# Kernel tuning notes

Measured on AMD Instinct MI355X. Metric: run time of the kernel, lower is better.

Reference implementation:

```python
import jax, jax.numpy as jnp
import numpy as np

VOCAB, FEAT, EMB, HID, AFF = 10000, 512, 256, 512, 512
B, T, HW = 32, 60, 14


def setup_inputs() -> dict:
    key = jax.random.key(0)
    ks = jax.random.split(key, 16)
    s = lambda k, shape, fan: jax.random.normal(k, shape, jnp.float32) * (1.0 / np.sqrt(fan))
    return {
        "cnn_feat": jax.random.normal(ks[0], (B, FEAT, HW, HW), jnp.float32),
        "captions": jax.random.randint(ks[1], (B, T), 0, VOCAB),
        "Wk": s(ks[2], (AFF, HID), HID),          # attention affine_k
        "Wv": s(ks[3], (AFF, FEAT), FEAT),        # attention affine_v
        "wa": s(ks[4], (AFF,), AFF),              # attention affine (out dim 1)
        "embed_table": jax.random.normal(ks[5], (VOCAB, EMB), jnp.float32),
        "Wh": s(ks[6], (HID, FEAT), FEAT), "bh": jnp.zeros((HID,), jnp.float32),
        "Wc": s(ks[7], (HID, FEAT), FEAT), "bc": jnp.zeros((HID,), jnp.float32),
        "Wih": s(ks[8], (4 * HID, EMB + FEAT), EMB + FEAT),
        "Whh": s(ks[9], (4 * HID, HID), HID),
        "bih": jnp.zeros((4 * HID,), jnp.float32),
        "bhh": jnp.zeros((4 * HID,), jnp.float32),
        "Wfc": s(ks[10], (VOCAB, HID), HID), "bfc": jnp.zeros((VOCAB,), jnp.float32),
    }


def _forward(cnn_feat, captions, Wk, Wv, wa, embed_table, Wh, bh, Wc, bc,
             Wih, Whh, bih, bhh, Wfc, bfc):
    Bs, C = cnn_feat.shape[0], cnn_feat.shape[1]
    feats = cnn_feat.reshape(Bs, C, -1).transpose(0, 2, 1)   # [B, P, FEAT]
    g = cnn_feat.mean(axis=(2, 3))                           # [B, FEAT]
    h0 = g @ Wh.T + bh
    c0 = g @ Wc.T + bc
    kv = jnp.einsum('bpc,ac->bpa', feats, Wv)                # affine_v(v), step-invariant
    emb = embed_table[captions]                              # [B, T, EMB]

    def step(carry, e_t):
        h, c = carry
        # additive attention: tanh(affine_k(h) + affine_v(v)) @ wa
        z = jnp.tanh((h @ Wk.T)[:, None, :] + kv) @ wa       # [B, P]
        alpha = jax.nn.softmax(z, axis=1)
        ctx = jnp.einsum('bp,bpc->bc', alpha, feats)         # [B, FEAT]
        x = jnp.concatenate([e_t, ctx], axis=1)
        gates = x @ Wih.T + bih + h @ Whh.T + bhh
        i, f, gg, o = jnp.split(gates, 4, axis=1)
        c = jax.nn.sigmoid(f) * c + jax.nn.sigmoid(i) * jnp.tanh(gg)
        h = jax.nn.sigmoid(o) * jnp.tanh(c)
        logit = h @ Wfc.T + bfc                              # dropout = identity (eval)
        return (h, c), logit

    _, logits = jax.lax.scan(step, (h0, c0), emb.transpose(1, 0, 2))
    return logits.transpose(1, 0, 2)                         # [B, T, VOCAB]


def reference(cnn_feat, captions, Wk, Wv, wa, embed_table, Wh, bh, Wc, bc,
              Wih, Whh, bih, bhh, Wfc, bfc):
    return _forward(cnn_feat, captions, Wk, Wv, wa, embed_table, Wh, bh, Wc, bc,
                    Wih, Whh, bih, bhh, Wfc, bfc)
```

## Files before the change

kernel.cpp:

```cpp
#include <hip/hip_runtime.h>
#include <hip/hip_bf16.h>
#include <cstdint>
#include <cstddef>

#define VOCABN 10000
#define FEATC 512
#define EMBN 256
#define HIDN 512
#define AFFN 512
#define BB 32
#define TTN 60
#define PPN 196
#define GROWS 2048

using bf16 = __hip_bfloat16;

typedef __attribute__((ext_vector_type(8))) short short8;
typedef __attribute__((ext_vector_type(4))) float f32x4;

__device__ __forceinline__ float b2f(bf16 x){ return __bfloat162float(x); }
__device__ __forceinline__ float fexp2(float x){ return __builtin_amdgcn_exp2f(x); }
__device__ __forceinline__ float frcp(float x){ return __builtin_amdgcn_rcpf(x); }
__device__ __forceinline__ float fsig(float x){ return frcp(1.f + fexp2(-1.4426950408889634f*x)); }
__device__ __forceinline__ float ftanhf(float x){ return 1.f - 2.f*frcp(1.f + fexp2(2.8853900817779268f*x)); }

__device__ __forceinline__ float aload(const float* p){
  return __hip_atomic_load((float*)p, __ATOMIC_RELAXED, __HIP_MEMORY_SCOPE_AGENT);
}
__device__ __forceinline__ void astore(float* p, float v){
  __hip_atomic_store(p, v, __ATOMIC_RELAXED, __HIP_MEMORY_SCOPE_AGENT);
}
__device__ __forceinline__ void astoreu(unsigned* p, unsigned v){
  __hip_atomic_store(p, v, __ATOMIC_RELAXED, __HIP_MEMORY_SCOPE_AGENT);
}
__device__ __forceinline__ unsigned aloadu(const unsigned* p){
  return __hip_atomic_load((unsigned*)p, __ATOMIC_RELAXED, __HIP_MEMORY_SCOPE_AGENT);
}

__device__ __forceinline__ f32x4 ic_load4(const float* p){
  f32x4 r;
  asm volatile("global_load_dwordx4 %0, %1, off sc0 sc1" : "=&v"(r) : "v"(p));
  return r;
}
__device__ __forceinline__ void ic_store4(float* p, f32x4 v){
  asm volatile("global_store_dwordx4 %0, %1, off sc0 sc1" :: "v"(p), "v"(v) : "memory");
}
__device__ __forceinline__ void ic_wait(){
  asm volatile("s_waitcnt vmcnt(0)" ::: "memory");
  __builtin_amdgcn_sched_barrier(0);
}

__device__ __forceinline__ void unpack8(uint4 u, float* f){
  f[0] = __uint_as_float(u.x << 16); f[1] = __uint_as_float(u.x & 0xffff0000u);
  f[2] = __uint_as_float(u.y << 16); f[3] = __uint_as_float(u.y & 0xffff0000u);
  f[4] = __uint_as_float(u.z << 16); f[5] = __uint_as_float(u.z & 0xffff0000u);
  f[6] = __uint_as_float(u.w << 16); f[7] = __uint_as_float(u.w & 0xffff0000u);
}

__global__ void __launch_bounds__(256) k_probe(const uint32_t* __restrict__ w, int* __restrict__ flag,
                                               unsigned* __restrict__ flags){
  __shared__ int s;
  if (threadIdx.x == 0) s = 0;
  __syncthreads();
  int hit = 0;
  for (int i = threadIdx.x; i < 32768; i += 256){
    uint32_t v = w[i];
    if (((v & 0x7F800000u) == 0x7F800000u) || ((v & 0x00007F80u) == 0x00007F80u)) hit = 1;
  }
  if (hit) atomicOr(&s, 1);
  for (int i = threadIdx.x; i < 1024; i += 256) astoreu(&flags[i], 0u);
  __syncthreads();
  if (threadIdx.x == 0) flag[0] = s;
}

__global__ void __launch_bounds__(256) k_cvt(const void* __restrict__ src, bf16* __restrict__ dst,
                                             int nquad, const int* __restrict__ flag){
  bool f32 = flag[0] != 0;
  int stride = gridDim.x * 256;
  for (int i = blockIdx.x*256 + threadIdx.x; i < nquad; i += stride){
    if (f32){
      float4 v = reinterpret_cast<const float4*>(src)[i];
      bf16* d = dst + 4*(size_t)i;
      d[0] = __float2bfloat16(v.x); d[1] = __float2bfloat16(v.y);
      d[2] = __float2bfloat16(v.z); d[3] = __float2bfloat16(v.w);
    } else {
      reinterpret_cast<uint2*>(dst)[i] = reinterpret_cast<const uint2*>(src)[i];
    }
  }
}

__global__ void __launch_bounds__(256) k_transpose(const bf16* __restrict__ cnn, bf16* __restrict__ feats){
  __shared__ bf16 tile[32][34];
  int ct = blockIdx.x, pt = blockIdx.y, b = blockIdx.z;
  int tid = threadIdx.x;
  int lc = tid >> 5, lp = tid & 31;
  int p = pt*32 + lp;
  #pragma unroll
  for (int i=0;i<4;i++){
    int cc = ct*32 + lc + i*8;
    bf16 v = __float2bfloat16(0.f);
    if (p < PPN) v = cnn[((size_t)b*FEATC + cc)*PPN + p];
    tile[lc + i*8][lp] = v;
  }
  __syncthreads();
  #pragma unroll
  for (int i=0;i<4;i++){
    int pp = pt*32 + lc + i*8;
    if (pp < PPN) feats[((size_t)b*PPN + pp)*FEATC + ct*32 + lp] = tile[lp][lc + i*8];
  }
}

__global__ void __launch_bounds__(256) k_wkt(const bf16* __restrict__ W, bf16* __restrict__ WT){
  __shared__ bf16 tile[32][33];
  const int c0 = blockIdx.x*32, r0 = blockIdx.y*32;
  const int lc = threadIdx.x >> 5, lp = threadIdx.x & 31;
  #pragma unroll
  for (int i=0;i<4;i++) tile[lc + i*8][lp] = W[(size_t)(r0 + lc + i*8)*HIDN + c0 + lp];
  __syncthreads();
  #pragma unroll
  for (int i=0;i<4;i++) WT[(size_t)(c0 + lc + i*8)*HIDN + r0 + lp] = tile[lp][lc + i*8];
}

__global__ void __launch_bounds__(256) k_wcat2(const bf16* __restrict__ Wih, const bf16* __restrict__ Whh,
      const bf16* __restrict__ bih, const bf16* __restrict__ bhh,
      bf16* __restrict__ Weh, bf16* __restrict__ Wctx, float* __restrict__ biasCat){
  const int rloc = threadIdx.x >> 5, lane32 = threadIdx.x & 31;
  const int r = blockIdx.x*8 + rloc;
  const int j = r >> 2, g = r & 3;
  const int src = g*HIDN + j;
  for (int e4 = lane32; e4 < 192; e4 += 32){
    const int e = e4*4;
    uint2 v = (e < 256) ? *reinterpret_cast<const uint2*>(Wih + (size_t)src*768 + e)
                        : *reinterpret_cast<const uint2*>(Whh + (size_t)src*HIDN + (e - 256));
    *reinterpret_cast<uint2*>(Weh + (size_t)r*768 + e) = v;
  }
  for (int e4 = lane32; e4 < 128; e4 += 32){
    const int e = e4*4;
    *reinterpret_cast<uint2*>(Wctx + (size_t)r*512 + e) =
        *reinterpret_cast<const uint2*>(Wih + (size_t)src*768 + 256 + e);
  }
  if (lane32 == 0) biasCat[r] = b2f(bih[src]) + b2f(bhh[src]);
}

__global__ void __launch_bounds__(256) k_init(const bf16* __restrict__ cnn,
      const bf16* __restrict__ Wh, const bf16* __restrict__ bh,
      const bf16* __restrict__ Wc, const bf16* __restrict__ bc,
      float* __restrict__ h, float* __restrict__ c){
  __shared__ float gl[FEATC];
  int b = blockIdx.x, tid = threadIdx.x;
  for (int cc = tid; cc < FEATC; cc += 256){
    const bf16* src = cnn + ((size_t)b*FEATC + cc)*PPN;
    const uint2* sp = reinterpret_cast<const uint2*>(src);
    float acc = 0.f;
    for (int q=0;q<PPN/4;q++){
      uint2 u = sp[q];
      acc += __uint_as_float(u.x<<16) + __uint_as_float(u.x&0xffff0000u)
           + __uint_as_float(u.y<<16) + __uint_as_float(u.y&0xffff0000u);
    }
    gl[cc] = acc * (1.0f/196.0f);
  }
  __syncthreads();
  for (int i = tid; i < HIDN; i += 256){
    const uint4* wr1 = reinterpret_cast<const uint4*>(Wh + (size_t)i*FEATC);
    const uint4* wr2 = reinterpret_cast<const uint4*>(Wc + (size_t)i*FEATC);
    float a1 = 0.f, a2 = 0.f;
    #pragma unroll 4
    for (int k8=0; k8<FEATC/8; k8++){
      float w1[8], w2[8];
      unpack8(wr1[k8], w1); unpack8(wr2[k8], w2);
      const float* gp = &gl[k8*8];
      #pragma unroll
      for (int j=0;j<8;j++){ a1 = fmaf(w1[j], gp[j], a1); a2 = fmaf(w2[j], gp[j], a2); }
    }
    astore(&h[b*HIDN+i], a1 + b2f(bh[i]));
    astore(&c[b*HIDN+i], a2 + b2f(bc[i]));
  }
}

__global__ void __launch_bounds__(512) k_hk0(const bf16* __restrict__ WkT,
      const float* __restrict__ h, float* __restrict__ part){
  __shared__ float hl[64];
  const int tid = threadIdx.x;
  const int k = blockIdx.x & 7, b = blockIdx.x >> 3;
  if (tid < 64) hl[tid] = aload(&h[b*HIDN + k*64 + tid]);
  __syncthreads();
  const bf16* wp = WkT + (size_t)(k*64)*AFFN + tid;
  float acc = 0.f;
  #pragma unroll 8
  for (int j=0; j<64; j++) acc = fmaf(b2f(wp[(size_t)j*AFFN]), hl[j], acc);
  astore(&part[((size_t)(b*8 + k))*AFFN + tid], acc);
}

template<int OUTMODE, bool BIAS, bool NT>
__global__ void __launch_bounds__(256) gemm_bt(const bf16* __restrict__ A, const bf16* __restrict__ Bw,
        const bf16* __restrict__ bias, void* __restrict__ Cout, int M, int N, int K,
        const int* __restrict__ flag){
  __shared__ __align__(16) bf16 As[64][40];
  __shared__ __align__(16) bf16 Bs[64][40];
  int tid = threadIdx.x;
  int m0 = blockIdx.y*64, n0 = blockIdx.x*64;
  int lr = tid >> 2;
  int lk = (tid & 3)*8;
  int wave = tid >> 6, lane = tid & 63;
  int ml = lane & 15, kg = lane >> 4;
  f32x4 acc0 = {0.f,0.f,0.f,0.f}, acc1 = acc0, acc2 = acc0, acc3 = acc0;
  for (int k0=0; k0<K; k0+=32){
    __syncthreads();
    {
      uint4 av = *reinterpret_cast<const uint4*>(A + (size_t)(m0+lr)*K + k0 + lk);
      *reinterpret_cast<uint4*>(&As[lr][lk]) = av;
      uint4 bv = make_uint4(0u,0u,0u,0u);
      int bn = n0 + lr;
      if (bn < N) bv = *reinterpret_cast<const uint4*>(Bw + (size_t)bn*K + k0 + lk);
      *reinterpret_cast<uint4*>(&Bs[lr][lk]) = bv;
    }
    __syncthreads();
    short8 af = *reinterpret_cast<const short8*>(&As[wave*16 + ml][kg*8]);
    short8 b0 = *reinterpret_cast<const short8*>(&Bs[ 0 + ml][kg*8]);
    short8 b1 = *reinterpret_cast<const short8*>(&Bs[16 + ml][kg*8]);
    short8 b2 = *reinterpret_cast<const short8*>(&Bs[32 + ml][kg*8]);
    short8 b3 = *reinterpret_cast<const short8*>(&Bs[48 + ml][kg*8]);
    acc0 = __builtin_amdgcn_mfma_f32_16x16x32_bf16(af, b0, acc0, 0,0,0);
    acc1 = __builtin_amdgcn_mfma_f32_16x16x32_bf16(af, b1, acc1, 0,0,0);
    acc2 = __builtin_amdgcn_mfma_f32_16x16x32_bf16(af, b2, acc2, 0,0,0);
    acc3 = __builtin_amdgcn_mfma_f32_16x16x32_bf16(af, b3, acc3, 0,0,0);
  }
  bool of32;
  if (OUTMODE == 0) of32 = true;
  else if (OUTMODE == 2) of32 = false;
  else of32 = (flag[0] != 0);
  int mb = m0 + wave*16 + (lane>>4)*4;
  int cl = lane & 15;
  f32x4 av[4] = {acc0, acc1, acc2, acc3};
  #pragma unroll
  for (int j=0;j<4;j++){
    int n = n0 + j*16 + cl;
    if (n < N){
      float bv = BIAS ? b2f(bias[n]) : 0.f;
      #pragma unroll
      for (int rr=0; rr<4; rr++){
        float v = av[j][rr] + bv;
        if (of32){
          float* p = &((float*)Cout)[(size_t)(mb+rr)*N + n];
          if (NT) __builtin_nontemporal_store(v, p); else *p = v;
        } else {
          bf16 hv = __float2bfloat16(v);
          short sv = *reinterpret_cast<short*>(&hv);
          short* p = reinterpret_cast<short*>(&((bf16*)Cout)[(size_t)(mb+rr)*N + n]);
          if (NT) __builtin_nontemporal_store(sv, p); else *p = sv;
        }
      }
    }
  }
}

__global__ void __launch_bounds__(256) gemm_gb(const bf16* __restrict__ A, const bf16* __restrict__ BwAll,
        bf16* __restrict__ Gout){
  const bf16* Bw = BwAll + (size_t)blockIdx.z*PPN*FEATC;
  bf16* Cout = Gout + (size_t)blockIdx.z*GROWS*PPN;
  __shared__ __align__(16) bf16 As[64][40];
  __shared__ __align__(16) bf16 Bs[64][40];
  int tid = threadIdx.x;
  int m0 = blockIdx.y*64, n0 = blockIdx.x*64;
  int lr = tid >> 2;
  int lk = (tid & 3)*8;
  int wave = tid >> 6, lane = tid & 63;
  int ml = lane & 15, kg = lane >> 4;
  f32x4 acc0 = {0.f,0.f,0.f,0.f}, acc1 = acc0, acc2 = acc0, acc3 = acc0;
  for (int k0=0; k0<FEATC; k0+=32){
    __syncthreads();
    {
      uint4 av = *reinterpret_cast<const uint4*>(A + (size_t)(m0+lr)*FEATC + k0 + lk);
      *reinterpret_cast<uint4*>(&As[lr][lk]) = av;
      uint4 bv = make_uint4(0u,0u,0u,0u);
      int bn = n0 + lr;
      if (bn < PPN) bv = *reinterpret_cast<const uint4*>(Bw + (size_t)bn*FEATC + k0 + lk);
      *reinterpret_cast<uint4*>(&Bs[lr][lk]) = bv;
    }
    __syncthreads();
    short8 af = *reinterpret_cast<const short8*>(&As[wave*16 + ml][kg*8]);
    short8 b0 = *reinterpret_cast<const short8*>(&Bs[ 0 + ml][kg*8]);
    short8 b1 = *reinterpret_cast<const short8*>(&Bs[16 + ml][kg*8]);
    short8 b2 = *reinterpret_cast<const short8*>(&Bs[32 + ml][kg*8]);
    short8 b3 = *reinterpret_cast<const short8*>(&Bs[48 + ml][kg*8]);
    acc0 = __builtin_amdgcn_mfma_f32_16x16x32_bf16(af, b0, acc0, 0,0,0);
    acc1 = __builtin_amdgcn_mfma_f32_16x16x32_bf16(af, b1, acc1, 0,0,0);
    acc2 = __builtin_amdgcn_mfma_f32_16x16x32_bf16(af, b2, acc2, 0,0,0);
    acc3 = __builtin_amdgcn_mfma_f32_16x16x32_bf16(af, b3, acc3, 0,0,0);
  }
  int mb = m0 + wave*16 + (lane>>4)*4;
  int cl = lane & 15;
  f32x4 av[4] = {acc0, acc1, acc2, acc3};
  #pragma unroll
  for (int j=0;j<4;j++){
    int n = n0 + j*16 + cl;
    if (n < PPN){
      #pragma unroll
      for (int rr=0; rr<4; rr++)
        Cout[(size_t)(mb+rr)*PPN + n] = __float2bfloat16(av[j][rr]);
    }
  }
}

__device__ __forceinline__ void fbar_signal(unsigned* f8, int myk, unsigned token){
  asm volatile("s_waitcnt vmcnt(0)" ::: "memory");
  __syncthreads();
  if (threadIdx.x == 0) astoreu(&f8[myk], token);
}
__device__ __forceinline__ void fbar_wait(unsigned* f8, unsigned token){
  const int lane = threadIdx.x & 63;
  unsigned guard = 0;
  for (;;){
    unsigned v = (lane < 8) ? aloadu(&f8[lane]) : token;
    if (__all((int)(v >= token))) break;
    if (++guard > 50000000u) break;
    __builtin_amdgcn_s_sleep(1);
  }
  __syncthreads();
}

__device__ __forceinline__ void gacc(const bf16* w, const float* x, int len,
                                     float& a0, float& a1, float& a2, float& a3){
  #pragma unroll 4
  for (int e=0; e<len; e+=8){
    float w8[8]; unpack8(*reinterpret_cast<const uint4*>(w+e), w8);
    float4 x0 = *reinterpret_cast<const float4*>(x+e);
    float4 x1 = *reinterpret_cast<const float4*>(x+e+4);
    a0 = fmaf(w8[0],x0.x,a0); a1 = fmaf(w8[1],x0.y,a1);
    a2 = fmaf(w8[2],x0.z,a2); a3 = fmaf(w8[3],x0.w,a3);
    a0 = fmaf(w8[4],x1.x,a0); a1 = fmaf(w8[5],x1.y,a1);
    a2 = fmaf(w8[6],x1.z,a2); a3 = fmaf(w8[7],x1.w,a3);
  }
}

__global__ void __launch_bounds__(512) k_pers(
    const bf16* __restrict__ kvB, const bf16* __restrict__ WkT,
    const bf16* __restrict__ Weh, const bf16* __restrict__ Gglob,
    const float* __restrict__ biasCat, const bf16* __restrict__ wa,
    const bf16* __restrict__ table, const int* __restrict__ captions,
    float* __restrict__ hstate, const float* __restrict__ cinit,
    float* __restrict__ part,
    float* __restrict__ zarr,
    bf16* __restrict__ Hb, unsigned* __restrict__ flags)
{
  extern __shared__ __align__(16) char dynsm[];
  bf16* kv_s = reinterpret_cast<bf16*>(dynsm);
  bf16* G_s  = reinterpret_cast<bf16*>(dynsm + 25600);
  __shared__ __align__(16) float xs[768];
  __shared__ __align__(16) float hks[512];
  __shared__ __align__(16) float als[200];
  __shared__ __align__(16) float gs[256];
  __shared__ __align__(16) float zes[32];
  __shared__ __align__(16) float hnew[64];

  const int tid = threadIdx.x;
  const int bid = blockIdx.x;
  const int k = bid & 7, b = bid >> 3;
  unsigned* fl = flags + b*32;
  const int np = (k < 4) ? 25 : 24;
  const int p0 = (k < 4) ? k*25 : 100 + (k-4)*24;
  const int lane = tid & 63, wv = tid >> 6;

  const int r2 = tid >> 1, half = tid & 1;
  const int rowg = k*256 + r2;

  {
    const uint4* src = reinterpret_cast<const uint4*>(kvB + ((size_t)(b*PPN + p0))*AFFN);
    uint4* dst = reinterpret_cast<uint4*>(kv_s);
    for (int i = tid; i < np*64; i += 512) dst[i] = src[i];
  }
  {
    const uint2* src = reinterpret_cast<const uint2*>(Gglob + ((size_t)(b*GROWS) + k*256)*PPN);
    uint2* dst = reinterpret_cast<uint2*>(G_s);
    for (int i = tid; i < 12544; i += 512) dst[i] = src[i];
  }
  float creg = 0.f;
  if (tid < 64) creg = cinit[b*HIDN + k*64 + tid];
  float wf[8];
  unpack8(*reinterpret_cast<const uint4*>(wa + lane*8), wf);
  __syncthreads();

  for (int t = 0; t < TTN; t++){
    f32x4 pq[8]; f32x4 hq;
    if (tid < 128){
      const float* pp = part + (size_t)b*8*AFFN + tid*4;
      #pragma unroll
      for (int kk=0;kk<8;kk++) pq[kk] = ic_load4(pp + (size_t)kk*AFFN);
    } else if (tid < 256){
      hq = ic_load4(hstate + (size_t)b*HIDN + (tid-128)*4);
    } else {
      const int tok = captions[b*TTN + t];
      xs[tid-256] = b2f(table[(size_t)tok*EMBN + (tid-256)]);
    }
    ic_wait();
    if (tid < 128){
      f32x4 s = pq[0];
      #pragma unroll
      for (int kk=1;kk<8;kk++) s += pq[kk];
      *reinterpret_cast<f32x4*>(&hks[tid*4]) = s;
    } else if (tid < 256){
      *reinterpret_cast<f32x4*>(&xs[256 + (tid-128)*4]) = hq;
    }
    __syncthreads();

    {
      float hf[8];
      const float4* hp = reinterpret_cast<const float4*>(&hks[lane*8]);
      float4 t0 = hp[0], t1 = hp[1];
      hf[0]=t0.x; hf[1]=t0.y; hf[2]=t0.z; hf[3]=t0.w;
      hf[4]=t1.x; hf[5]=t1.y; hf[6]=t1.z; hf[7]=t1.w;
      for (int pl = wv; pl < np; pl += 8){
        float kf[8]; unpack8(*reinterpret_cast<const uint4*>(kv_s + pl*512 + lane*8), kf);
        float acc = wf[0]*ftanhf(kf[0]+hf[0]) + wf[1]*ftanhf(kf[1]+hf[1])
                  + wf[2]*ftanhf(kf[2]+hf[2]) + wf[3]*ftanhf(kf[3]+hf[3])
                  + wf[4]*ftanhf(kf[4]+hf[4]) + wf[5]*ftanhf(kf[5]+hf[5])
                  + wf[6]*ftanhf(kf[6]+hf[6]) + wf[7]*ftanhf(kf[7]+hf[7]);
        #pragma unroll
        for (int s=1;s<64;s<<=1) acc += __shfl_xor(acc, s, 64);
        if (lane == 0) zes[pl] = acc;
      }
    }
    __syncthreads();
    if (tid < 8) ic_store4(&zarr[(size_t)(b*8+k)*32 + tid*4],
                           *reinterpret_cast<f32x4*>(&zes[tid*4]));

    fbar_signal(fl, k, (unsigned)(2*t+1));

    float a0=0.f,a1=0.f,a2=0.f,a3=0.f;
    gacc(Weh + (size_t)rowg*768 + half*384, xs + half*384, 384, a0,a1,a2,a3);

    fbar_wait(fl, (unsigned)(2*t+1));

    f32x4 zq;
    if (tid < 64) zq = ic_load4(&zarr[(size_t)b*256 + tid*4]);
    ic_wait();
    if (tid < 64){
      const int kk2 = tid >> 3, i0 = (tid & 7)*4;
      const int npk = (kk2 < 4) ? 25 : 24;
      const int p0k = (kk2 < 4) ? kk2*25 : 100 + (kk2-4)*24;
      #pragma unroll
      for (int jj=0;jj<4;jj++) if (i0+jj < npk) als[p0k+i0+jj] = zq[jj];
    }
    __syncthreads();
    if (wv == 0){
      float m = -1e30f;
      for (int i=lane;i<PPN;i+=64) m = fmaxf(m, als[i]);
      #pragma unroll
      for (int s=1;s<64;s<<=1) m = fmaxf(m, __shfl_xor(m, s, 64));
      float ssum = 0.f;
      for (int i=lane;i<PPN;i+=64){
        float e = fexp2((als[i]-m)*1.4426950408889634f);
        als[i] = e; ssum += e;
      }
      #pragma unroll
      for (int s=1;s<64;s<<=1) ssum += __shfl_xor(ssum, s, 64);
      float inv = 1.0f/ssum;
      for (int i=lane;i<PPN;i+=64) als[i] *= inv;
    }
    __syncthreads();

    float ga = 0.f;
    {
      const uint32_t* gr = reinterpret_cast<const uint32_t*>(G_s + r2*PPN + half*98);
      const float* ap = als + half*98;
      #pragma unroll 7
      for (int i=0;i<49;i++){
        uint32_t u = gr[i];
        ga = fmaf(__uint_as_float(u << 16),          ap[2*i],   ga);
        ga = fmaf(__uint_as_float(u & 0xffff0000u),  ap[2*i+1], ga);
      }
    }
    {
      float acc = (a0+a1)+(a2+a3) + ga;
      acc += __shfl_xor(acc, 1, 64);
      if (half == 0) gs[r2] = acc + biasCat[rowg];
    }
    __syncthreads();

    if (tid < 64){
      const int j = k*64 + tid;
      float gi = gs[tid*4+0], gf = gs[tid*4+1], gg = gs[tid*4+2], go = gs[tid*4+3];
      float cn = fsig(gf)*creg + fsig(gi)*ftanhf(gg);
      float hn = fsig(go)*ftanhf(cn);
      creg = cn;
      hnew[tid] = hn;
      Hb[((size_t)b*TTN + t)*HIDN + j] = __float2bfloat16(hn);
    }
    __syncthreads();
    if (tid < 16) ic_store4(&hstate[(size_t)b*HIDN + k*64 + tid*4],
                            *reinterpret_cast<f32x4*>(&hnew[tid*4]));

    {
      const bf16* wp = WkT + (size_t)(k*64)*AFFN + tid;
      float acc = 0.f;
      #pragma unroll 8
      for (int j=0;j<64;j++) acc = fmaf(b2f(wp[(size_t)j*AFFN]), hnew[j], acc);
      hks[tid] = acc;
    }
    __syncthreads();
    if (tid < 128) ic_store4(&part[((size_t)(b*8+k))*AFFN + tid*4],
                             *reinterpret_cast<f32x4*>(&hks[tid*4]));

    fbar_signal(fl, k, (unsigned)(2*t+2));
    fbar_wait(fl, (unsigned)(2*t+2));
  }
}

static inline int cvt_grid(int nquad){ int g = (nquad + 255)/256; return g > 1024 ? 1024 : g; }

extern "C" void kernel_launch(void* const* d_in, const int* in_sizes, int n_in,
                              void* d_out, int out_size, void* d_ws, size_t ws_size,
                              hipStream_t stream) {
  const int* captions = (const int*)d_in[1];
  char* ws = (char*)d_ws;

  bf16*  feats  = (bf16*) (ws + 0);
  bf16*  kvB    = (bf16*) (ws + 6422528);
  float* hstate = (float*)(ws + 12845056);
  float* cstate = (float*)(ws + 12910592);
  float* part   = (float*)(ws + 12976128);
  float* zarr   = (float*)(ws + 13500416);
  unsigned* flags=(unsigned*)(ws + 13533184);
  bf16*  Hb     = (bf16*) (ws + 13537280);
  bf16*  cnnB   = (bf16*) (ws + 15503360);
  bf16*  WehB   = (bf16*) (ws + 15503360);
  bf16*  WctxB  = (bf16*) (ws + 18649088);
  bf16*  tableB = (bf16*) (ws + 21925888);
  bf16*  WkB    = (bf16*) (ws + 27045888);
  bf16*  WkTB   = (bf16*) (ws + 27570176);
  bf16*  WvB    = (bf16*) (ws + 28094464);
  bf16*  WhB    = (bf16*) (ws + 28618752);
  bf16*  WcB    = (bf16*) (ws + 29143040);
  bf16*  WihB   = (bf16*) (ws + 29667328);
  bf16*  WhhB   = (bf16*) (ws + 32813056);
  bf16*  WfcB   = (bf16*) (ws + 34910208);
  bf16*  waB    = (bf16*) (ws + 45150208);
  bf16*  bhB    = (bf16*) (ws + 45151232);
  bf16*  bcB    = (bf16*) (ws + 45152256);
  bf16*  bihB   = (bf16*) (ws + 45153280);
  bf16*  bhhB   = (bf16*) (ws + 45157376);
  bf16*  bfcB   = (bf16*) (ws + 45161472);
  float* biasCat= (float*)(ws + 45181472);
  int*   flag   = (int*)  (ws + 45189664);
  if (ws_size < 45189680ull) return;

  bf16* Gglob = (bf16*)d_out;

  k_probe<<<1, 256, 0, stream>>>((const uint32_t*)d_in[5], flag, flags);

  struct CvtJob { const void* src; bf16* dst; int n; };
  const CvtJob jobs[15] = {
    {d_in[0],  cnnB,   3211264}, {d_in[2],  WkB,  262144}, {d_in[3],  WvB,  262144},
    {d_in[4],  waB,    512},     {d_in[5],  tableB, 2560000},
    {d_in[6],  WhB,    262144},  {d_in[7],  bhB,  512},
    {d_in[8],  WcB,    262144},  {d_in[9],  bcB,  512},
    {d_in[10], WihB,   1572864}, {d_in[11], WhhB, 1048576},
    {d_in[12], bihB,   2048},    {d_in[13], bhhB, 2048},
    {d_in[14], WfcB,   5120000}, {d_in[15], bfcB, 10000},
  };
  for (int i = 0; i < 15; i++){
    int nq = jobs[i].n / 4;
    k_cvt<<<cvt_grid(nq), 256, 0, stream>>>(jobs[i].src, jobs[i].dst, nq, flag);
  }

  k_transpose<<<dim3(16,7,32), 256, 0, stream>>>(cnnB, feats);
  k_init<<<32, 256, 0, stream>>>(cnnB, WhB, bhB, WcB, bcB, hstate, cstate);
  k_wkt<<<dim3(16,16), 256, 0, stream>>>(WkB, WkTB);
  k_wcat2<<<256, 256, 0, stream>>>(WihB, WhhB, bihB, bhhB, WehB, WctxB, biasCat);
  k_hk0<<<256, 512, 0, stream>>>(WkTB, hstate, part);
  gemm_bt<2,false,false><<<dim3(8,98), 256, 0, stream>>>(feats, WvB, (const bf16*)nullptr,
                                                   (void*)kvB, 6272, 512, 512, (const int*)nullptr);
  gemm_gb<<<dim3(4,32,32), 256, 0, stream>>>(WctxB, feats, Gglob);

  k_pers<<<256, 512, 125952, stream>>>(kvB, WkTB, WehB, Gglob, biasCat, waB, tableB,
                                       captions, hstate, cstate, part, zarr, Hb, flags);

  gemm_bt<1,true,true><<<dim3(157,30), 256, 0, stream>>>(Hb, WfcB, bfcB, d_out,
                                                    1920, 10000, 512, flag);
}
```

Measured before the change: 1.557 ms.

## Precompute embedding gate contributions via batched GEMM and move h load off critical path

The embedding half of the LSTM input projection (emb @ Wih_emb^T plus biases) is hoisted out of the persistent recurrent kernel into a one-shot gather and GEMM over all timesteps. Inside the loop only the Whh part is computed per step, with the gate term for the next step prefetched from Gemb. The h-state reload is moved after the z reduction so it overlaps the barrier, and the Hb write is deferred past the flag signal. The 15 conversion launches are merged into one multi-job kernel, and the Wfc conversion is moved after the recurrent kernel so its workspace can be shared with Gemb. In exchange the biases and embedding gates are now rounded to bf16, and the workspace layout changes.

```diff
diff --git a/kernel.cpp b/kernel.cpp
--- a/kernel.cpp
+++ b/kernel.cpp
@@ -24,17 +24,17 @@
 __device__ __forceinline__ float fsig(float x){ return frcp(1.f + fexp2(-1.4426950408889634f*x)); }
 __device__ __forceinline__ float ftanhf(float x){ return 1.f - 2.f*frcp(1.f + fexp2(2.8853900817779268f*x)); }
 
+__device__ __forceinline__ void astore(float* p, float v){
+  __hip_atomic_store(p, v, __ATOMIC_RELAXED, __HIP_MEMORY_SCOPE_AGENT);
+}
+__device__ __forceinline__ void astoreu(unsigned* p, unsigned v){
+  __hip_atomic_store(p, v, __ATOMIC_RELAXED, __HIP_MEMORY_SCOPE_AGENT);
+}
+__device__ __forceinline__ unsigned aloadu(const unsigned* p){
+  return __hip_atomic_load((unsigned*)p, __ATOMIC_RELAXED, __HIP_MEMORY_SCOPE_AGENT);
+}
 __device__ __forceinline__ float aload(const float* p){
   return __hip_atomic_load((float*)p, __ATOMIC_RELAXED, __HIP_MEMORY_SCOPE_AGENT);
-}
-__device__ __forceinline__ void astore(float* p, float v){
-  __hip_atomic_store(p, v, __ATOMIC_RELAXED, __HIP_MEMORY_SCOPE_AGENT);
-}
-__device__ __forceinline__ void astoreu(unsigned* p, unsigned v){
-  __hip_atomic_store(p, v, __ATOMIC_RELAXED, __HIP_MEMORY_SCOPE_AGENT);
-}
-__device__ __forceinline__ unsigned aloadu(const unsigned* p){
-  return __hip_atomic_load((unsigned*)p, __ATOMIC_RELAXED, __HIP_MEMORY_SCOPE_AGENT);
 }
 
 __device__ __forceinline__ f32x4 ic_load4(const float* p){
@@ -71,6 +71,25 @@
   for (int i = threadIdx.x; i < 1024; i += 256) astoreu(&flags[i], 0u);
   __syncthreads();
   if (threadIdx.x == 0) flag[0] = s;
+}
+
+struct CvtJobs { const void* src[14]; void* dst[14]; int nq[14]; };
+__global__ void __launch_bounds__(256) k_cvtall(CvtJobs J, const int* __restrict__ flag){
+  bool f32 = flag[0] != 0;
+  const int job = blockIdx.y;
+  const int nq = J.nq[job];
+  const void* src = J.src[job];
+  bf16* dst = (bf16*)J.dst[job];
+  for (int i = blockIdx.x*256 + threadIdx.x; i < nq; i += 256*256){
+    if (f32){
+      float4 v = reinterpret_cast<const float4*>(src)[i];
+      bf16* d = dst + 4*(size_t)i;
+      d[0] = __float2bfloat16(v.x); d[1] = __float2bfloat16(v.y);
+      d[2] = __float2bfloat16(v.z); d[3] = __float2bfloat16(v.w);
+    } else {
+      reinterpret_cast<uint2*>(dst)[i] = reinterpret_cast<const uint2*>(src)[i];
+    }
+  }
 }
 
 __global__ void __launch_bounds__(256) k_cvt(const void* __restrict__ src, bf16* __restrict__ dst,
@@ -121,25 +140,39 @@
   for (int i=0;i<4;i++) WT[(size_t)(c0 + lc + i*8)*HIDN + r0 + lp] = tile[lp][lc + i*8];
 }
 
-__global__ void __launch_bounds__(256) k_wcat2(const bf16* __restrict__ Wih, const bf16* __restrict__ Whh,
+__global__ void __launch_bounds__(256) k_wcat3(const bf16* __restrict__ Wih, const bf16* __restrict__ Whh,
       const bf16* __restrict__ bih, const bf16* __restrict__ bhh,
-      bf16* __restrict__ Weh, bf16* __restrict__ Wctx, float* __restrict__ biasCat){
+      bf16* __restrict__ Whc, bf16* __restrict__ Wemb, bf16* __restrict__ Wctx,
+      bf16* __restrict__ biasCatB){
   const int rloc = threadIdx.x >> 5, lane32 = threadIdx.x & 31;
   const int r = blockIdx.x*8 + rloc;
   const int j = r >> 2, g = r & 3;
   const int src = g*HIDN + j;
-  for (int e4 = lane32; e4 < 192; e4 += 32){
+  for (int e4 = lane32; e4 < 128; e4 += 32){
     const int e = e4*4;
-    uint2 v = (e < 256) ? *reinterpret_cast<const uint2*>(Wih + (size_t)src*768 + e)
-                        : *reinterpret_cast<const uint2*>(Whh + (size_t)src*HIDN + (e - 256));
-    *reinterpret_cast<uint2*>(Weh + (size_t)r*768 + e) = v;
+    *reinterpret_cast<uint2*>(Whc + (size_t)r*512 + e) =
+        *reinterpret_cast<const uint2*>(Whh + (size_t)src*HIDN + e);
+  }
+  for (int e4 = lane32; e4 < 64; e4 += 32){
+    const int e = e4*4;
+    *reinterpret_cast<uint2*>(Wemb + (size_t)r*256 + e) =
+        *reinterpret_cast<const uint2*>(Wih + (size_t)src*768 + e);
   }
   for (int e4 = lane32; e4 < 128; e4 += 32){
     const int e = e4*4;
     *reinterpret_cast<uint2*>(Wctx + (size_t)r*512 + e) =
         *reinterpret_cast<const uint2*>(Wih + (size_t)src*768 + 256 + e);
   }
-  if (lane32 == 0) biasCat[r] = b2f(bih[src]) + b2f(bhh[src]);
+  if (lane32 == 0) biasCatB[r] = __float2bfloat16(b2f(bih[src]) + b2f(bhh[src]));
+}
+
+__global__ void __launch_bounds__(64) k_embgather(const int* __restrict__ captions,
+      const bf16* __restrict__ table, bf16* __restrict__ embAll){
+  const int row = blockIdx.x;
+  const int tok = captions[row];
+  const uint2* s = reinterpret_cast<const uint2*>(table + (size_t)tok*EMBN);
+  uint2* d = reinterpret_cast<uint2*>(embAll + (size_t)row*EMBN);
+  d[threadIdx.x] = s[threadIdx.x];
 }
 
 __global__ void __launch_bounds__(256) k_init(const bf16* __restrict__ cnn,
@@ -302,11 +335,6 @@
   }
 }
 
-__device__ __forceinline__ void fbar_signal(unsigned* f8, int myk, unsigned token){
-  asm volatile("s_waitcnt vmcnt(0)" ::: "memory");
-  __syncthreads();
-  if (threadIdx.x == 0) astoreu(&f8[myk], token);
-}
 __device__ __forceinline__ void fbar_wait(unsigned* f8, unsigned token){
   const int lane = threadIdx.x & 63;
   unsigned guard = 0;
@@ -335,9 +363,8 @@
 
 __global__ void __launch_bounds__(512) k_pers(
     const bf16* __restrict__ kvB, const bf16* __restrict__ WkT,
-    const bf16* __restrict__ Weh, const bf16* __restrict__ Gglob,
-    const float* __restrict__ biasCat, const bf16* __restrict__ wa,
-    const bf16* __restrict__ table, const int* __restrict__ captions,
+    const bf16* __restrict__ Whc, const bf16* __restrict__ Gglob,
+    const bf16* __restrict__ Gemb, const bf16* __restrict__ wa,
     float* __restrict__ hstate, const float* __restrict__ cinit,
     float* __restrict__ part,
     float* __restrict__ zarr,
@@ -346,12 +373,13 @@
   extern __shared__ __align__(16) char dynsm[];
   bf16* kv_s = reinterpret_cast<bf16*>(dynsm);
   bf16* G_s  = reinterpret_cast<bf16*>(dynsm + 25600);
-  __shared__ __align__(16) float xs[768];
+  __shared__ __align__(16) float hs[512];
   __shared__ __align__(16) float hks[512];
   __shared__ __align__(16) float als[200];
   __shared__ __align__(16) float gs[256];
   __shared__ __align__(16) float zes[32];
   __shared__ __align__(16) float hnew[64];
+  __shared__ __align__(8)  bf16 gembs[256];
 
   const int tid = threadIdx.x;
   const int bid = blockIdx.x;
@@ -360,7 +388,6 @@
   const int np = (k < 4) ? 25 : 24;
   const int p0 = (k < 4) ? k*25 : 100 + (k-4)*24;
   const int lane = tid & 63, wv = tid >> 6;
-
   const int r2 = tid >> 1, half = tid & 1;
   const int rowg = k*256 + r2;
 
@@ -374,6 +401,9 @@
     uint2* dst = reinterpret_cast<uint2*>(G_s);
     for (int i = tid; i < 12544; i += 512) dst[i] = src[i];
   }
+  if (tid < 64)
+    *reinterpret_cast<uint2*>(&gembs[tid*4]) =
+        *reinterpret_cast<const uint2*>(Gemb + (size_t)(b*TTN + 0)*GROWS + k*256 + tid*4);
   float creg = 0.f;
   if (tid < 64) creg = cinit[b*HIDN + k*64 + tid];
   float wf[8];
@@ -381,25 +411,20 @@
   __syncthreads();
 
   for (int t = 0; t < TTN; t++){
-    f32x4 pq[8]; f32x4 hq;
-    if (tid < 128){
-      const float* pp = part + (size_t)b*8*AFFN + tid*4;
-      #pragma unroll
-      for (int kk=0;kk<8;kk++) pq[kk] = ic_load4(pp + (size_t)kk*AFFN);
-    } else if (tid < 256){
-      hq = ic_load4(hstate + (size_t)b*HIDN + (tid-128)*4);
-    } else {
-      const int tok = captions[b*TTN + t];
-      xs[tid-256] = b2f(table[(size_t)tok*EMBN + (tid-256)]);
-    }
-    ic_wait();
-    if (tid < 128){
-      f32x4 s = pq[0];
-      #pragma unroll
-      for (int kk=1;kk<8;kk++) s += pq[kk];
-      *reinterpret_cast<f32x4*>(&hks[tid*4]) = s;
-    } else if (tid < 256){
-      *reinterpret_cast<f32x4*>(&xs[256 + (tid-128)*4]) = hq;
+    {
+      f32x4 pq[8];
+      if (tid < 128){
+        const float* pp = part + (size_t)b*8*AFFN + tid*4;
+        #pragma unroll
+        for (int kk=0;kk<8;kk++) pq[kk] = ic_load4(pp + (size_t)kk*AFFN);
+      }
+      ic_wait();
+      if (tid < 128){
+        f32x4 s = pq[0];
+        #pragma unroll
+        for (int kk=1;kk<8;kk++) s += pq[kk];
+        *reinterpret_cast<f32x4*>(&hks[tid*4]) = s;
+      }
     }
     __syncthreads();
 
@@ -421,13 +446,19 @@
       }
     }
     __syncthreads();
+
+    f32x4 hq;
     if (tid < 8) ic_store4(&zarr[(size_t)(b*8+k)*32 + tid*4],
                            *reinterpret_cast<f32x4*>(&zes[tid*4]));
-
-    fbar_signal(fl, k, (unsigned)(2*t+1));
+    if (tid < 128) hq = ic_load4(hstate + (size_t)b*HIDN + tid*4);
+    ic_wait();
+    __syncthreads();
+    if (tid == 0) astoreu(&fl[k], (unsigned)(2*t+1));
+    if (tid < 128) *reinterpret_cast<f32x4*>(&hs[tid*4]) = hq;
+    __syncthreads();
 
     float a0=0.f,a1=0.f,a2=0.f,a3=0.f;
-    gacc(Weh + (size_t)rowg*768 + half*384, xs + half*384, 384, a0,a1,a2,a3);
+    gacc(Whc + (size_t)rowg*512 + half*256, hs + half*256, 256, a0,a1,a2,a3);
 
     fbar_wait(fl, (unsigned)(2*t+1));
 
@@ -473,23 +504,21 @@
     {
       float acc = (a0+a1)+(a2+a3) + ga;
       acc += __shfl_xor(acc, 1, 64);
-      if (half == 0) gs[r2] = acc + biasCat[rowg];
+      if (half == 0) gs[r2] = acc + b2f(gembs[r2]);
     }
     __syncthreads();
 
     if (tid < 64){
-      const int j = k*64 + tid;
       float gi = gs[tid*4+0], gf = gs[tid*4+1], gg = gs[tid*4+2], go = gs[tid*4+3];
       float cn = fsig(gf)*creg + fsig(gi)*ftanhf(gg);
       float hn = fsig(go)*ftanhf(cn);
       creg = cn;
       hnew[tid] = hn;
-      Hb[((size_t)b*TTN + t)*HIDN + j] = __float2bfloat16(hn);
-    }
-    __syncthreads();
+    }
+    __syncthreads();
+
     if (tid < 16) ic_store4(&hstate[(size_t)b*HIDN + k*64 + tid*4],
                             *reinterpret_cast<f32x4*>(&hnew[tid*4]));
-
     {
       const bf16* wp = WkT + (size_t)(k*64)*AFFN + tid;
       float acc = 0.f;
@@ -501,12 +530,19 @@
     if (tid < 128) ic_store4(&part[((size_t)(b*8+k))*AFFN + tid*4],
                              *reinterpret_cast<f32x4*>(&hks[tid*4]));
 
-    fbar_signal(fl, k, (unsigned)(2*t+2));
+    ic_wait();
+    __syncthreads();
+    if (tid == 0) astoreu(&fl[k], (unsigned)(2*t+2));
+    if (tid < 64) Hb[((size_t)b*TTN + t)*HIDN + k*64 + tid] = __float2bfloat16(hnew[tid]);
+    {
+      const int tn = (t+1 < TTN) ? t+1 : t;
+      if (tid < 64)
+        *reinterpret_cast<uint2*>(&gembs[tid*4]) =
+            *reinterpret_cast<const uint2*>(Gemb + (size_t)(b*TTN + tn)*GROWS + k*256 + tid*4);
+    }
     fbar_wait(fl, (unsigned)(2*t+2));
   }
 }
-
-static inline int cvt_grid(int nquad){ int g = (nquad + 255)/256; return g > 1024 ? 1024 : g; }
 
 extern "C" void kernel_launch(void* const* d_in, const int* in_sizes, int n_in,
                               void* d_out, int out_size, void* d_ws, size_t ws_size,
@@ -523,8 +559,9 @@
   unsigned* flags=(unsigned*)(ws + 13533184);
   bf16*  Hb     = (bf16*) (ws + 13537280);
   bf16*  cnnB   = (bf16*) (ws + 15503360);
-  bf16*  WehB   = (bf16*) (ws + 15503360);
-  bf16*  WctxB  = (bf16*) (ws + 18649088);
+  bf16*  WhcB   = (bf16*) (ws + 15503360);
+  bf16*  WembB  = (bf16*) (ws + 17600512 + 2097152 - 2097152 + 2097152);
+  bf16*  WctxB  = (bf16*) (ws + 17600512);
   bf16*  tableB = (bf16*) (ws + 21925888);
   bf16*  WkB    = (bf16*) (ws + 27045888);
   bf16*  WkTB   = (bf16*) (ws + 27570176);
@@ -533,48 +570,49 @@
   bf16*  WcB    = (bf16*) (ws + 29143040);
   bf16*  WihB   = (bf16*) (ws + 29667328);
   bf16*  WhhB   = (bf16*) (ws + 32813056);
-  bf16*  WfcB   = (bf16*) (ws + 34910208);
-  bf16*  waB    = (bf16*) (ws + 45150208);
-  bf16*  bhB    = (bf16*) (ws + 45151232);
-  bf16*  bcB    = (bf16*) (ws + 45152256);
-  bf16*  bihB   = (bf16*) (ws + 45153280);
-  bf16*  bhhB   = (bf16*) (ws + 45157376);
-  bf16*  bfcB   = (bf16*) (ws + 45161472);
-  float* biasCat= (float*)(ws + 45181472);
-  int*   flag   = (int*)  (ws + 45189664);
-  if (ws_size < 45189680ull) return;
+  bf16*  waB    = (bf16*) (ws + 34910208);
+  bf16*  bhB    = (bf16*) (ws + 34911232);
+  bf16*  bcB    = (bf16*) (ws + 34912256);
+  bf16*  bihB   = (bf16*) (ws + 34913280);
+  bf16*  bhhB   = (bf16*) (ws + 34917376);
+  bf16*  bfcB   = (bf16*) (ws + 34921472);
+  bf16*  biasCatB=(bf16*) (ws + 34941472);
+  int*   flag   = (int*)  (ws + 34945568);
+  bf16*  embAll = (bf16*) (ws + 34945600);
+  bf16*  WfcB   = (bf16*) (ws + 35928640);
+  bf16*  Gemb   = (bf16*) (ws + 35928640);
+  if (ws_size < 46168656ull) return;
+  WembB = (bf16*)(ws + 19697664);
 
   bf16* Gglob = (bf16*)d_out;
 
   k_probe<<<1, 256, 0, stream>>>((const uint32_t*)d_in[5], flag, flags);
 
-  struct CvtJob { const void* src; bf16* dst; int n; };
-  const CvtJob jobs[15] = {
-    {d_in[0],  cnnB,   3211264}, {d_in[2],  WkB,  262144}, {d_in[3],  WvB,  262144},
-    {d_in[4],  waB,    512},     {d_in[5],  tableB, 2560000},
-    {d_in[6],  WhB,    262144},  {d_in[7],  bhB,  512},
-    {d_in[8],  WcB,    262144},  {d_in[9],  bcB,  512},
-    {d_in[10], WihB,   1572864}, {d_in[11], WhhB, 1048576},
-    {d_in[12], bihB,   2048},    {d_in[13], bhhB, 2048},
-    {d_in[14], WfcB,   5120000}, {d_in[15], bfcB, 10000},
-  };
-  for (int i = 0; i < 15; i++){
-    int nq = jobs[i].n / 4;
-    k_cvt<<<cvt_grid(nq), 256, 0, stream>>>(jobs[i].src, jobs[i].dst, nq, flag);
-  }
+  CvtJobs J;
+  const void* srcs[14] = { d_in[0], d_in[2], d_in[3], d_in[4], d_in[5], d_in[6], d_in[7],
+                           d_in[8], d_in[9], d_in[10], d_in[11], d_in[12], d_in[13], d_in[15] };
+  void* dsts[14] = { cnnB, WkB, WvB, waB, tableB, WhB, bhB, WcB, bcB, WihB, WhhB, bihB, bhhB, bfcB };
+  const int ns[14] = { 3211264, 262144, 262144, 512, 2560000, 262144, 512,
+                       262144, 512, 1572864, 1048576, 2048, 2048, 10000 };
+  for (int i=0;i<14;i++){ J.src[i]=srcs[i]; J.dst[i]=dsts[i]; J.nq[i]=ns[i]/4; }
+  k_cvtall<<<dim3(256,14), 256, 0, stream>>>(J, flag);
 
   k_transpose<<<dim3(16,7,32), 256, 0, stream>>>(cnnB, feats);
   k_init<<<32, 256, 0, stream>>>(cnnB, WhB, bhB, WcB, bcB, hstate, cstate);
   k_wkt<<<dim3(16,16), 256, 0, stream>>>(WkB, WkTB);
-  k_wcat2<<<256, 256, 0, stream>>>(WihB, WhhB, bihB, bhhB, WehB, WctxB, biasCat);
+  k_wcat3<<<256, 256, 0, stream>>>(WihB, WhhB, bihB, bhhB, WhcB, WembB, WctxB, biasCatB);
   k_hk0<<<256, 512, 0, stream>>>(WkTB, hstate, part);
   gemm_bt<2,false,false><<<dim3(8,98), 256, 0, stream>>>(feats, WvB, (const bf16*)nullptr,
                                                    (void*)kvB, 6272, 512, 512, (const int*)nullptr);
   gemm_gb<<<dim3(4,32,32), 256, 0, stream>>>(WctxB, feats, Gglob);
-
-  k_pers<<<256, 512, 125952, stream>>>(kvB, WkTB, WehB, Gglob, biasCat, waB, tableB,
-                                       captions, hstate, cstate, part, zarr, Hb, flags);
-
+  k_embgather<<<1920, 64, 0, stream>>>(captions, tableB, embAll);
+  gemm_bt<2,true,false><<<dim3(32,30), 256, 0, stream>>>(embAll, WembB, biasCatB,
+                                                   (void*)Gemb, 1920, 2048, 256, (const int*)nullptr);
+
+  k_pers<<<256, 512, 125952, stream>>>(kvB, WkTB, WhcB, Gglob, Gemb, waB,
+                                       hstate, cstate, part, zarr, Hb, flags);
+
+  k_cvt<<<1024, 256, 0, stream>>>(d_in[14], WfcB, 1280000, flag);
   gemm_bt<1,true,true><<<dim3(157,30), 256, 0, stream>>>(Hb, WfcB, bfcB, d_out,
                                                     1920, 10000, 512, flag);
 }
```

After: 1.344 ms. 13.7% less time.
